# Performance work log

Hardware: AMD Instinct MI355X
Metric: run time of the kernel (lower is better)

Reference implementation:

```python
import jax, jax.numpy as jnp
import numpy as np

NUM_CLASSES = 19
IGNORE = 255
KLD_MARGIN = 3.0
DEC = 0.01
BOT_EPS, TOP_EPS = 1e-4, 1.0
# eight-corner neighbor offsets (size=1), order matches AAF layers.eightcorner_activation
EDGE_OFFS = ((-1, -1), (-1, 0), (-1, 1), (0, -1), (0, 1), (1, -1), (1, 0), (1, 1))


def _shift(x, dy, dx, pad_val):
    # Shift along H,W (axes 1,2): out[:, y, x] = x[:, y+dy, x+dx], padded with pad_val.
    pads = [(0, 0), (1, 1), (1, 1)] + [(0, 0)] * (x.ndim - 3)
    xp = jnp.pad(x, pads, constant_values=pad_val)
    h, w = x.shape[1], x.shape[2]
    return xp[:, 1 + dy:1 + dy + h, 1 + dx:1 + dx + w]


def _resize_bilinear_ac(x, oh, ow):
    # torch F.interpolate(mode='bilinear', align_corners=True) on NCHW.
    n, c, h, w = x.shape
    ys = jnp.linspace(0.0, h - 1.0, oh)
    xs = jnp.linspace(0.0, w - 1.0, ow)
    y0 = jnp.floor(ys).astype(jnp.int32); y1 = jnp.minimum(y0 + 1, h - 1)
    x0 = jnp.floor(xs).astype(jnp.int32); x1 = jnp.minimum(x0 + 1, w - 1)
    wy = (ys - y0).astype(x.dtype)[None, None, :, None]
    wx = (xs - x0).astype(x.dtype)[None, None, None, :]
    rows = x[:, :, y0, :] * (1.0 - wy) + x[:, :, y1, :] * wy  # (N,C,oh,W)
    return rows[:, :, :, x0] * (1.0 - wx) + rows[:, :, :, x1] * wx  # (N,C,oh,ow)


def setup_inputs() -> dict:
    key = jax.random.key(0)
    k1, k2 = jax.random.split(key)
    preds = jax.random.normal(k1, (2, NUM_CLASSES, 64, 64), dtype=jnp.float32)
    targets = jax.random.randint(k2, (2, 512, 512), 0, NUM_CLASSES, dtype=jnp.int32)
    w_edge = jnp.zeros((1, 1, 1, NUM_CLASSES, 1, 3), dtype=jnp.float32)
    w_not_edge = jnp.zeros((1, 1, 1, NUM_CLASSES, 1, 3), dtype=jnp.float32)
    return {"preds": preds, "targets": targets, "w_edge": w_edge, "w_not_edge": w_not_edge}


def reference(preds, targets, w_edge, w_not_edge):
    h, w = targets.shape[1], targets.shape[2]
    pred = _resize_bilinear_ac(preds, h, w)          # (N,C,H,W)
    prob = jax.nn.softmax(pred, axis=1)
    prob = jnp.transpose(prob, (0, 2, 3, 1))          # (N,H,W,C) NHWC layout used by AAF layers

    labels = targets                                  # (N,H,W)
    ign = labels == IGNORE
    one_label = jnp.where(ign, 0, labels)
    ohl = jax.nn.one_hot(one_label, NUM_CLASSES, dtype=jnp.float32)  # (N,H,W,C)
    ohl = jnp.where(ign[..., None], float(IGNORE), ohl)

    # edge/non-edge class weights: softmax over last dim, take index 0 -> (1,1,1,C,1)
    w_e = jax.nn.softmax(w_edge, axis=-1)[..., 0]
    w_ne = jax.nn.softmax(w_not_edge, axis=-1)[..., 0]

    # ignores_from_label: bidirectional ignore mask, neighbor order is reversed offsets
    ignore_c = labels > NUM_CLASSES - 1               # (N,H,W)
    ignore8 = jnp.stack([_shift(ignore_c, -dy, -dx, True) | ignore_c for dy, dx in EDGE_OFFS], axis=-1)
    not_ignore = ~ignore8[:, :, :, None, :]           # (N,H,W,1,8)

    # edges_from_label: neighbor label (padded with ignore_class) differs from center
    edge8 = jnp.stack([_shift(ohl, dy, dx, float(IGNORE)) != ohl for dy, dx in EDGE_OFFS], axis=-1)  # (N,H,W,C,8)
    edge = edge8 & not_ignore
    not_edge = (~edge) & not_ignore

    # eightcorner_activation on probabilities (zero padded)
    probs_paired = jnp.stack([_shift(prob, dy, dx, 0.0) for dy, dx in EDGE_OFFS], axis=-1)  # (N,H,W,C,8)
    p = prob[..., None]                               # (N,H,W,C,1)
    pc = jnp.clip(p, BOT_EPS, TOP_EPS)
    npc = jnp.clip(1.0 - p, BOT_EPS, TOP_EPS)
    ppc = jnp.clip(probs_paired, BOT_EPS, TOP_EPS)
    nppc = jnp.clip(1.0 - probs_paired, BOT_EPS, TOP_EPS)

    # binary KL divergence per class/neighbor
    kldiv = ppc * jnp.log(ppc / pc) + nppc * jnp.log(nppc / npc)  # (N,H,W,C,8)

    # per-pixel class weights: sum_c w[c]*one_hot[c] -> (N,H,W,1,1)
    we_map = jnp.sum(w_e * ohl[..., None], axis=3, keepdims=True)
    wne_map = jnp.sum(w_ne * ohl[..., None], axis=3, keepdims=True)

    edge_loss = jnp.maximum(0.0, KLD_MARGIN - kldiv) * we_map
    not_edge_loss = kldiv * wne_map

    # torch.mean over gathered nonzero indices == masked sum / count
    e_cnt = jnp.maximum(jnp.sum(edge), 1).astype(jnp.float32)
    ne_cnt = jnp.maximum(jnp.sum(not_edge), 1).astype(jnp.float32)
    e_mean = jnp.sum(jnp.where(edge, edge_loss, 0.0)) / e_cnt
    ne_mean = jnp.sum(jnp.where(not_edge, not_edge_loss, 0.0)) / ne_cnt

    return e_mean * 1.0 * DEC + ne_mean * 1.0 * DEC
```

## Files before the change

### kernel.cpp

```cpp
#include <hip/hip_runtime.h>
#include <stdint.h>


#define NC 19
#define HH 512
#define WW 512
#define NB 2
#define TS 16
#define HS 18
#define HP (HS * HS)
#define NPAIR 10
#define ATRS 22
#define DRS 11
#define PS 25
#define NBLK (NB * (HH / TS) * (WW / TS))
#define LOGEPS -9.210340371976182f

typedef _Float16 f16x2 __attribute__((ext_vector_type(2)));

#if __has_builtin(__builtin_amdgcn_fdot2)
#define FDOT2(a, b, c) __builtin_amdgcn_fdot2((a), (b), (c), false)
#else
#define FDOT2(a, b, c) fmaf((float)(a)[1], (float)(b)[1], fmaf((float)(a)[0], (float)(b)[0], (c)))
#endif

struct Part { float es, ns; int ec, nc; };

union U32F2 { uint32_t u; f16x2 h; };
__device__ __forceinline__ uint32_t bc_u32(f16x2 v) { U32F2 x; x.h = v; return x.u; }
__device__ __forceinline__ f16x2 bc_h2(uint32_t v) { U32F2 x; x.u = v; return x.h; }
__device__ __forceinline__ float extf(f16x2 v, int h) { return h ? (float)v[1] : (float)v[0]; }

__global__ __launch_bounds__(256, 3) void k_fused(const float* __restrict__ preds,
                                                  const int* __restrict__ targets,
                                                  const float* __restrict__ w_edge,
                                                  const float* __restrict__ w_not_edge,
                                                  Part* __restrict__ pb) {
    __shared__ __align__(16) uint32_t AT[HP * ATRS];
    __shared__ uint32_t DP[HP * DRS];
    __shared__ int   TG[HP];
    __shared__ float swe[NC], swn[NC];
    __shared__ float patch[NC * PS];

    const int tid = threadIdx.x;
    const int bx = blockIdx.x, by = blockIdx.y, n = blockIdx.z;

    if (tid < NC) {
        {
            float a = w_edge[tid * 3 + 0], b = w_edge[tid * 3 + 1], c = w_edge[tid * 3 + 2];
            float m = fmaxf(a, fmaxf(b, c));
            float ea = __expf(a - m), eb = __expf(b - m), ec = __expf(c - m);
            swe[tid] = ea / (ea + eb + ec);
        }
        {
            float a = w_not_edge[tid * 3 + 0], b = w_not_edge[tid * 3 + 1], c = w_not_edge[tid * 3 + 2];
            float m = fmaxf(a, fmaxf(b, c));
            float ea = __expf(a - m), eb = __expf(b - m), ec = __expf(c - m);
            swn[tid] = ea / (ea + eb + ec);
        }
    }

    const int* tg = targets + (n << 18);
    const float* pbase = preds + (size_t)n * NC * 4096;

    const int yT = max(by * TS - 1, 0), xL = max(bx * TS - 1, 0);
    const int y0b = (yT * 63) / 511, x0b = (xL * 63) / 511;
    for (int t = tid; t < NC * PS; t += 256) {
        const int c = t / PS, r = t - c * PS;
        const int ry = r / 5, rx = r - ry * 5;
        const int sy = min(y0b + ry, 63), sx = min(x0b + rx, 63);
        patch[t] = pbase[c * 4096 + (sy << 6) + sx];
    }
    __syncthreads();

    for (int i = tid; i < HP; i += 256) {
        const int hy = i / HS, hx = i - hy * HS;
        const int y = by * TS + hy - 1;
        const int x = bx * TS + hx - 1;
        _Float16 a16s[NPAIR * 2], d16s[NPAIR * 2], t16s[NPAIR * 2];
        if (((unsigned)y >= (unsigned)HH) | ((unsigned)x >= (unsigned)WW)) {
            TG[i] = 255;
            const _Float16 aP = (_Float16)1e-4f, dP = (_Float16)LOGEPS;
            const _Float16 tP = (_Float16)fmaf((float)aP, (float)dP, 0.0f);
#pragma unroll
            for (int c = 0; c < NC; ++c) { a16s[c] = aP; d16s[c] = dP; t16s[c] = tP; }
        } else {
            TG[i] = tg[(y << 9) + x];
            const float fy = (float)(y * 63) / 511.0f;
            const float fx = (float)(x * 63) / 511.0f;
            const int y0 = (int)fy, x0 = (int)fx;
            const float wy = fy - (float)y0, wx = fx - (float)x0;
            const int y1 = min(y0 + 1, 63), x1 = min(x0 + 1, 63);
            const float omwy = 1.0f - wy, omwx = 1.0f - wx;
            const int o00 = (y0 - y0b) * 5 + (x0 - x0b);
            const int o01 = (y0 - y0b) * 5 + (x1 - x0b);
            const int o10 = (y1 - y0b) * 5 + (x0 - x0b);
            const int o11 = (y1 - y0b) * 5 + (x1 - x0b);

            float v[NC], w[NC];
            float m = -1e30f;
#pragma unroll
            for (int c = 0; c < NC; ++c) {
                const float* pc_ = &patch[c * PS];
                const float a = pc_[o00] * omwy + pc_[o10] * wy;
                const float b = pc_[o01] * omwy + pc_[o11] * wy;
                const float vv = a * omwx + b * wx;
                v[c] = vv;
                m = fmaxf(m, vv);
            }
            float s = 0.0f;
#pragma unroll
            for (int c = 0; c < NC; ++c) { w[c] = __expf(v[c] - m); s += w[c]; }
            const float inv = 1.0f / s;
            const float lns = __logf(s) + m;
#pragma unroll
            for (int c = 0; c < NC; ++c) {
                const float p = w[c] * inv;
                const float la = fmaxf(v[c] - lns, LOGEPS);
                const float aa = fmaxf(p, 1e-4f);
                const float lb = __logf(fmaxf(1.0f - p, 1e-4f));
                const _Float16 a16 = (_Float16)aa;
                const _Float16 d16 = (_Float16)(la - lb);
                const _Float16 l16 = (_Float16)lb;
                a16s[c] = a16; d16s[c] = d16;
                t16s[c] = (_Float16)fmaf((float)a16, (float)d16, (float)l16);
            }
        }
        a16s[19] = (_Float16)0.0f; d16s[19] = (_Float16)0.0f; t16s[19] = (_Float16)0.0f;
#pragma unroll
        for (int j = 0; j < NPAIR; ++j) {
            f16x2 a2 = {a16s[2 * j], a16s[2 * j + 1]};
            f16x2 t2 = {t16s[2 * j], t16s[2 * j + 1]};
            f16x2 d2 = {d16s[2 * j], d16s[2 * j + 1]};
            uint2 wv; wv.x = bc_u32(a2); wv.y = bc_u32(t2);
            *reinterpret_cast<uint2*>(&AT[i * ATRS + 2 * j]) = wv;
            DP[i * DRS + j] = bc_u32(d2);
        }
    }
    __syncthreads();

    const int ty = tid >> 4, tx = tid & 15;
    const int hi = (ty + 1) * HS + (tx + 1);
    const int lab = TG[hi];
    const bool interior_blk = (bx > 0) & (bx < 31) & (by > 0) & (by < 31);

    float e_s = 0.0f, ne_s = 0.0f;
    int e_c = 0, ne_c = 0;
    const int DOFF[8] = {-HS - 1, -HS, -HS + 1, -1, 1, HS - 1, HS, HS + 1};
    const f16x2 one2 = {(_Float16)1.0f, (_Float16)1.0f};
    const f16x2 k32 = {(_Float16)3.0f, (_Float16)3.0f};
    const f16x2 z2 = {(_Float16)0.0f, (_Float16)0.0f};

    f16x2 Dh[NPAIR], Lh[NPAIR];
#pragma unroll
    for (int j = 0; j < NPAIR; ++j) {
        const uint2 rd = *reinterpret_cast<const uint2*>(&AT[hi * ATRS + 2 * j]);
        const f16x2 a2 = bc_h2(rd.x), t2 = bc_h2(rd.y);
        Dh[j] = bc_h2(DP[hi * DRS + j]);
        Lh[j] = t2 - a2 * Dh[j];
    }
    const int plab = lab >> 1, hlab = lab & 1;

    if (interior_blk) {
#pragma unroll
        for (int k = 0; k < 8; ++k) {
            const int np = hi + DOFF[k];
            const int nlab = TG[np];
            const int pn = nlab >> 1, hn = nlab & 1;
            const int wb = np * ATRS;
            float dot = 0.0f;
            f16x2 klLw = z2, klNw = z2;
#pragma unroll
            for (int j = 0; j < NPAIR; ++j) {
                const uint2 rd = *reinterpret_cast<const uint2*>(&AT[wb + 2 * j]);
                const f16x2 a2 = bc_h2(rd.x), t2 = bc_h2(rd.y);
                const f16x2 x2 = a2 * Dh[j] + Lh[j];
                const f16x2 kl2 = t2 - x2;
                dot = FDOT2(kl2, one2, dot);
                klLw = (j == plab) ? kl2 : klLw;
                klNw = (j == pn) ? kl2 : klNw;
            }
            const float klL = extf(klLw, hlab);
            const float klN = extf(klNw, hn);
            const bool df = (lab != nlab);
            const float w = df ? 1.0f : 0.0f;
            e_s = fmaf(w, fmaxf(3.0f - klL, 0.0f) + fmaxf(3.0f - klN, 0.0f), e_s);
            ne_s += dot - w * (klL + klN);
            e_c += df ? 2 : 0;
        }
        ne_c = 8 * NC - e_c;
        e_s *= swe[lab];
        ne_s *= swn[lab];
    } else if (lab <= NC - 1) {
#pragma unroll
        for (int k = 0; k < 8; ++k) {
            const int off = DOFF[k];
            const int rlab = TG[hi - off];
            const int np = hi + off;
            const int nlab = TG[np];
            const int pn = nlab >> 1, hn = nlab & 1;
            const int wb = np * ATRS;
            float dot = 0.0f, ekall = 0.0f;
            f16x2 klLw = z2, klNw = z2;
#pragma unroll
            for (int j = 0; j < NPAIR; ++j) {
                const uint2 rd = *reinterpret_cast<const uint2*>(&AT[wb + 2 * j]);
                const f16x2 a2 = bc_h2(rd.x), t2 = bc_h2(rd.y);
                const f16x2 x2 = a2 * Dh[j] + Lh[j];
                const f16x2 kl2 = t2 - x2;
                dot = FDOT2(kl2, one2, dot);
                f16x2 m2 = k32 - kl2;
                m2[0] = m2[0] > (_Float16)0.0f ? m2[0] : (_Float16)0.0f;
                m2[1] = m2[1] > (_Float16)0.0f ? m2[1] : (_Float16)0.0f;
                ekall = FDOT2(m2, one2, ekall);
                klLw = (j == plab) ? kl2 : klLw;
                klNw = (j == pn) ? kl2 : klNw;
            }
            const float klL = extf(klLw, hlab);
            const float klN = extf(klNw, hn);
            const bool isPad = (nlab == 255);
            const bool df = (lab != nlab) && !isPad;
            const float w = df ? 1.0f : 0.0f;
            const float ek_int = w * (fmaxf(3.0f - klL, 0.0f) + fmaxf(3.0f - klN, 0.0f));
            const float nk_int = dot - w * (klL + klN);
            const float ek_pad = ekall - 3.0f;
            const float ek_k = isPad ? ek_pad : ek_int;
            const float nk_k = isPad ? 0.0f : nk_int;
            const int pc = isPad ? NC : (df ? 2 : 0);
            const bool valid = (rlab <= NC - 1);
            const float vf = valid ? 1.0f : 0.0f;
            e_s = fmaf(vf, ek_k, e_s);
            ne_s = fmaf(vf, nk_k, ne_s);
            e_c += valid ? pc : 0;
            ne_c += valid ? (NC - pc) : 0;
        }
        e_s *= swe[lab];
        ne_s *= swn[lab];
    }

#pragma unroll
    for (int off = 32; off > 0; off >>= 1) {
        e_s  += __shfl_down(e_s, off, 64);
        ne_s += __shfl_down(ne_s, off, 64);
        e_c  += __shfl_down(e_c, off, 64);
        ne_c += __shfl_down(ne_c, off, 64);
    }
    __shared__ float r_es[4], r_ns[4];
    __shared__ int r_ec[4], r_nc[4];
    const int wid = tid >> 6, lane = tid & 63;
    if (lane == 0) { r_es[wid] = e_s; r_ns[wid] = ne_s; r_ec[wid] = e_c; r_nc[wid] = ne_c; }
    __syncthreads();
    if (tid == 0) {
        float tes = 0.0f, tns = 0.0f;
        int tec = 0, tnc = 0;
#pragma unroll
        for (int w = 0; w < 4; ++w) { tes += r_es[w]; tns += r_ns[w]; tec += r_ec[w]; tnc += r_nc[w]; }
        const int bid = (blockIdx.z * gridDim.y + blockIdx.y) * gridDim.x + blockIdx.x;
        pb[bid].es = tes; pb[bid].ns = tns; pb[bid].ec = tec; pb[bid].nc = tnc;
    }
}

__global__ __launch_bounds__(256) void k_final(const Part* __restrict__ pb,
                                               float* __restrict__ out) {
    const int tid = threadIdx.x;
    double es = 0.0, ns = 0.0;
    long long ec = 0, nc = 0;
    for (int i = tid; i < NBLK; i += 256) {
        es += (double)pb[i].es; ns += (double)pb[i].ns;
        ec += pb[i].ec; nc += pb[i].nc;
    }
#pragma unroll
    for (int off = 32; off > 0; off >>= 1) {
        es += __shfl_down(es, off, 64);
        ns += __shfl_down(ns, off, 64);
        ec += __shfl_down(ec, off, 64);
        nc += __shfl_down(nc, off, 64);
    }
    __shared__ double ses[4], sns[4];
    __shared__ long long sec[4], snc[4];
    const int wid = tid >> 6, lane = tid & 63;
    if (lane == 0) { ses[wid] = es; sns[wid] = ns; sec[wid] = ec; snc[wid] = nc; }
    __syncthreads();
    if (tid == 0) {
        double tes = 0.0, tns = 0.0;
        long long tec = 0, tnc = 0;
#pragma unroll
        for (int w = 0; w < 4; ++w) { tes += ses[w]; tns += sns[w]; tec += sec[w]; tnc += snc[w]; }
        double ecd = (double)tec; if (ecd < 1.0) ecd = 1.0;
        double ncd = (double)tnc; if (ncd < 1.0) ncd = 1.0;
        out[0] = (float)((tes / ecd) * 0.01 + (tns / ncd) * 0.01);
    }
}

extern "C" void kernel_launch(void* const* d_in, const int* in_sizes, int n_in,
                              void* d_out, int out_size, void* d_ws, size_t ws_size,
                              hipStream_t stream) {
    const float* preds      = (const float*)d_in[0];
    const int*   targets    = (const int*)d_in[1];
    const float* w_edge     = (const float*)d_in[2];
    const float* w_not_edge = (const float*)d_in[3];

    Part* pb = (Part*)d_ws;

    dim3 grid(WW / TS, HH / TS, NB);
    k_fused<<<grid, 256, 0, stream>>>(preds, targets, w_edge, w_not_edge, pb);
    k_final<<<1, 256, 0, stream>>>(pb, (float*)d_out);
}
```

Before: 104.0 us.

## Keep center pixel D/L in registers, drop DP shared array, raise occupancy

Each thread now computes its own center pixel's softmax and log terms and keeps the D and L halves in registers. Only the A/T pairs go to shared memory, so the DP shared array is removed. A 68-thread halo pass fills the border. The smaller shared footprint allows raising the launch-bounds occupancy hint from 3 to 5 blocks. The trade-offs are that the halo pass runs on only 68 of 256 threads, which adds a serialized tail, and that the new occupancy target puts more pressure on registers.

```diff
diff --git a/kernel.cpp b/kernel.cpp
--- a/kernel.cpp
+++ b/kernel.cpp
@@ -11,7 +11,6 @@
 #define HP (HS * HS)
 #define NPAIR 10
 #define ATRS 22
-#define DRS 11
 #define PS 25
 #define NBLK (NB * (HH / TS) * (WW / TS))
 #define LOGEPS -9.210340371976182f
@@ -31,16 +30,91 @@
 __device__ __forceinline__ f16x2 bc_h2(uint32_t v) { U32F2 x; x.u = v; return x.h; }
 __device__ __forceinline__ float extf(f16x2 v, int h) { return h ? (float)v[1] : (float)v[0]; }
 
-__global__ __launch_bounds__(256, 3) void k_fused(const float* __restrict__ preds,
+template <bool KEEP>
+__device__ __forceinline__ int pix_compute(const float* __restrict__ patch,
+                                           const int* __restrict__ tg,
+                                           int y, int x, int y0b, int x0b,
+                                           uint32_t* __restrict__ ATrow,
+                                           f16x2* Dh, f16x2* Lh) {
+    _Float16 a16s[NPAIR * 2], t16s[NPAIR * 2], d16s[NPAIR * 2], l16s[NPAIR * 2];
+    int lab;
+    if (((unsigned)y >= (unsigned)HH) | ((unsigned)x >= (unsigned)WW)) {
+        lab = 255;
+        const _Float16 aP = (_Float16)1e-4f, dP = (_Float16)LOGEPS;
+        const _Float16 tP = (_Float16)((float)aP * (float)dP);
+#pragma unroll
+        for (int c = 0; c < NC; ++c) {
+            a16s[c] = aP; d16s[c] = dP; l16s[c] = (_Float16)0.0f; t16s[c] = tP;
+        }
+    } else {
+        lab = tg[(y << 9) + x];
+        const float fy = (float)(y * 63) / 511.0f;
+        const float fx = (float)(x * 63) / 511.0f;
+        const int y0 = (int)fy, x0 = (int)fx;
+        const float wy = fy - (float)y0, wx = fx - (float)x0;
+        const int y1 = min(y0 + 1, 63), x1 = min(x0 + 1, 63);
+        const float omwy = 1.0f - wy, omwx = 1.0f - wx;
+        const int o00 = (y0 - y0b) * 5 + (x0 - x0b);
+        const int o01 = (y0 - y0b) * 5 + (x1 - x0b);
+        const int o10 = (y1 - y0b) * 5 + (x0 - x0b);
+        const int o11 = (y1 - y0b) * 5 + (x1 - x0b);
+
+        float v[NC], w[NC];
+        float m = -1e30f;
+#pragma unroll
+        for (int c = 0; c < NC; ++c) {
+            const float* pc_ = &patch[c * PS];
+            const float a = pc_[o00] * omwy + pc_[o10] * wy;
+            const float b = pc_[o01] * omwy + pc_[o11] * wy;
+            const float vv = a * omwx + b * wx;
+            v[c] = vv;
+            m = fmaxf(m, vv);
+        }
+        float s = 0.0f;
+#pragma unroll
+        for (int c = 0; c < NC; ++c) { w[c] = __expf(v[c] - m); s += w[c]; }
+        const float inv = 1.0f / s;
+        const float lns = __logf(s) + m;
+#pragma unroll
+        for (int c = 0; c < NC; ++c) {
+            const float p = w[c] * inv;
+            const float la = fmaxf(v[c] - lns, LOGEPS);
+            const float aa = fmaxf(p, 1e-4f);
+            const float lb = __logf(fmaxf(1.0f - p, 1e-4f));
+            const _Float16 a16 = (_Float16)aa;
+            const _Float16 d16 = (_Float16)(la - lb);
+            const _Float16 l16 = (_Float16)lb;
+            a16s[c] = a16; d16s[c] = d16; l16s[c] = l16;
+            t16s[c] = (_Float16)fmaf((float)a16, (float)d16, (float)l16);
+        }
+    }
+    a16s[19] = (_Float16)0.0f; t16s[19] = (_Float16)0.0f;
+    d16s[19] = (_Float16)0.0f; l16s[19] = (_Float16)0.0f;
+#pragma unroll
+    for (int j = 0; j < NPAIR; ++j) {
+        uint2 wv;
+        wv.x = bc_u32((f16x2){a16s[2 * j], a16s[2 * j + 1]});
+        wv.y = bc_u32((f16x2){t16s[2 * j], t16s[2 * j + 1]});
+        *reinterpret_cast<uint2*>(ATrow + 2 * j) = wv;
+        if (KEEP) {
+            Dh[j] = (f16x2){d16s[2 * j], d16s[2 * j + 1]};
+            Lh[j] = (f16x2){l16s[2 * j], l16s[2 * j + 1]};
+        }
+    }
+    return lab;
+}
+
+__global__ __launch_bounds__(256, 5) void k_fused(const float* __restrict__ preds,
                                                   const int* __restrict__ targets,
                                                   const float* __restrict__ w_edge,
                                                   const float* __restrict__ w_not_edge,
                                                   Part* __restrict__ pb) {
     __shared__ __align__(16) uint32_t AT[HP * ATRS];
-    __shared__ uint32_t DP[HP * DRS];
     __shared__ int   TG[HP];
     __shared__ float swe[NC], swn[NC];
     __shared__ float patch[NC * PS];
+    __shared__ float r_es[4], r_ns[4];
+    __shared__ int r_ec[4], r_nc[4];
 
     const int tid = threadIdx.x;
     const int bx = blockIdx.x, by = blockIdx.y, n = blockIdx.z;
@@ -73,75 +147,26 @@
     }
     __syncthreads();
 
-    for (int i = tid; i < HP; i += 256) {
-        const int hy = i / HS, hx = i - hy * HS;
-        const int y = by * TS + hy - 1;
-        const int x = bx * TS + hx - 1;
-        _Float16 a16s[NPAIR * 2], d16s[NPAIR * 2], t16s[NPAIR * 2];
-        if (((unsigned)y >= (unsigned)HH) | ((unsigned)x >= (unsigned)WW)) {
-            TG[i] = 255;
-            const _Float16 aP = (_Float16)1e-4f, dP = (_Float16)LOGEPS;
-            const _Float16 tP = (_Float16)fmaf((float)aP, (float)dP, 0.0f);
-#pragma unroll
-            for (int c = 0; c < NC; ++c) { a16s[c] = aP; d16s[c] = dP; t16s[c] = tP; }
-        } else {
-            TG[i] = tg[(y << 9) + x];
-            const float fy = (float)(y * 63) / 511.0f;
-            const float fx = (float)(x * 63) / 511.0f;
-            const int y0 = (int)fy, x0 = (int)fx;
-            const float wy = fy - (float)y0, wx = fx - (float)x0;
-            const int y1 = min(y0 + 1, 63), x1 = min(x0 + 1, 63);
-            const float omwy = 1.0f - wy, omwx = 1.0f - wx;
-            const int o00 = (y0 - y0b) * 5 + (x0 - x0b);
-            const int o01 = (y0 - y0b) * 5 + (x1 - x0b);
-            const int o10 = (y1 - y0b) * 5 + (x0 - x0b);
-            const int o11 = (y1 - y0b) * 5 + (x1 - x0b);
-
-            float v[NC], w[NC];
-            float m = -1e30f;
-#pragma unroll
-            for (int c = 0; c < NC; ++c) {
-                const float* pc_ = &patch[c * PS];
-                const float a = pc_[o00] * omwy + pc_[o10] * wy;
-                const float b = pc_[o01] * omwy + pc_[o11] * wy;
-                const float vv = a * omwx + b * wx;
-                v[c] = vv;
-                m = fmaxf(m, vv);
-            }
-            float s = 0.0f;
-#pragma unroll
-            for (int c = 0; c < NC; ++c) { w[c] = __expf(v[c] - m); s += w[c]; }
-            const float inv = 1.0f / s;
-            const float lns = __logf(s) + m;
-#pragma unroll
-            for (int c = 0; c < NC; ++c) {
-                const float p = w[c] * inv;
-                const float la = fmaxf(v[c] - lns, LOGEPS);
-                const float aa = fmaxf(p, 1e-4f);
-                const float lb = __logf(fmaxf(1.0f - p, 1e-4f));
-                const _Float16 a16 = (_Float16)aa;
-                const _Float16 d16 = (_Float16)(la - lb);
-                const _Float16 l16 = (_Float16)lb;
-                a16s[c] = a16; d16s[c] = d16;
-                t16s[c] = (_Float16)fmaf((float)a16, (float)d16, (float)l16);
-            }
-        }
-        a16s[19] = (_Float16)0.0f; d16s[19] = (_Float16)0.0f; t16s[19] = (_Float16)0.0f;
-#pragma unroll
-        for (int j = 0; j < NPAIR; ++j) {
-            f16x2 a2 = {a16s[2 * j], a16s[2 * j + 1]};
-            f16x2 t2 = {t16s[2 * j], t16s[2 * j + 1]};
-            f16x2 d2 = {d16s[2 * j], d16s[2 * j + 1]};
-            uint2 wv; wv.x = bc_u32(a2); wv.y = bc_u32(t2);
-            *reinterpret_cast<uint2*>(&AT[i * ATRS + 2 * j]) = wv;
-            DP[i * DRS + j] = bc_u32(d2);
-        }
-    }
-    __syncthreads();
-
     const int ty = tid >> 4, tx = tid & 15;
     const int hi = (ty + 1) * HS + (tx + 1);
-    const int lab = TG[hi];
+    f16x2 Dh[NPAIR], Lh[NPAIR];
+    const int lab = pix_compute<true>(patch, tg, by * TS + ty, bx * TS + tx,
+                                      y0b, x0b, &AT[hi * ATRS], Dh, Lh);
+    TG[hi] = lab;
+
+    if (tid < 68) {
+        int i;
+        if (tid < 18)      i = tid;
+        else if (tid < 36) i = 306 + (tid - 18);
+        else if (tid < 52) i = (tid - 35) * HS;
+        else               i = (tid - 51) * HS + 17;
+        const int hy = i / HS, hx = i - hy * HS;
+        const int lab2 = pix_compute<false>(patch, tg, by * TS + hy - 1, bx * TS + hx - 1,
+                                            y0b, x0b, &AT[i * ATRS], nullptr, nullptr);
+        TG[i] = lab2;
+    }
+    __syncthreads();
+
     const bool interior_blk = (bx > 0) & (bx < 31) & (by > 0) & (by < 31);
 
     float e_s = 0.0f, ne_s = 0.0f;
@@ -150,15 +175,6 @@
     const f16x2 one2 = {(_Float16)1.0f, (_Float16)1.0f};
     const f16x2 k32 = {(_Float16)3.0f, (_Float16)3.0f};
     const f16x2 z2 = {(_Float16)0.0f, (_Float16)0.0f};
-
-    f16x2 Dh[NPAIR], Lh[NPAIR];
-#pragma unroll
-    for (int j = 0; j < NPAIR; ++j) {
-        const uint2 rd = *reinterpret_cast<const uint2*>(&AT[hi * ATRS + 2 * j]);
-        const f16x2 a2 = bc_h2(rd.x), t2 = bc_h2(rd.y);
-        Dh[j] = bc_h2(DP[hi * DRS + j]);
-        Lh[j] = t2 - a2 * Dh[j];
-    }
     const int plab = lab >> 1, hlab = lab & 1;
 
     if (interior_blk) {
@@ -245,8 +261,6 @@
         e_c  += __shfl_down(e_c, off, 64);
         ne_c += __shfl_down(ne_c, off, 64);
     }
-    __shared__ float r_es[4], r_ns[4];
-    __shared__ int r_ec[4], r_nc[4];
     const int wid = tid >> 6, lane = tid & 63;
     if (lane == 0) { r_es[wid] = e_s; r_ns[wid] = ne_s; r_ec[wid] = e_c; r_nc[wid] = ne_c; }
     __syncthreads();
```

Result: faster. 99.50 us (-4.4%).
